# Performance work log

Measured on AMD Instinct MI355X. Metric: run time of the kernel, lower is better.

## Reference

```python
import jax, jax.numpy as jnp
import numpy as np
import math

B, S, D = 2, 2048, 2048
H = 16
HD = D // H          # 128
LAT = 512            # latent_dim


def setup_inputs() -> dict:
    key = jax.random.key(0)
    ks = jax.random.split(key, 8)
    x = jax.random.normal(ks[0], (B, S, D), dtype=jnp.float32)
    freqs = jax.random.uniform(ks[1], (S, HD // 2), dtype=jnp.float32) * (2 * math.pi)
    # additive causal mask: 0 on/below diagonal, -1e9 above
    causal = jnp.tril(jnp.ones((S, S), dtype=bool))
    mask = jnp.where(causal, 0.0, -1e9).astype(jnp.float32)
    sc = 0.02
    Wq = jax.random.normal(ks[2], (D, H * HD), dtype=jnp.float32) * sc
    Wdown = jax.random.normal(ks[3], (D, LAT), dtype=jnp.float32) * sc
    Wkup = jax.random.normal(ks[4], (LAT, H * HD), dtype=jnp.float32) * sc
    Wvup = jax.random.normal(ks[5], (LAT, H * HD), dtype=jnp.float32) * sc
    Wo = jax.random.normal(ks[6], (D, D), dtype=jnp.float32) * sc
    return {"x": x, "freqs": freqs, "mask": mask,
            "Wq": Wq, "Wdown": Wdown, "Wkup": Wkup, "Wvup": Wvup, "Wo": Wo}


def _apply_rope(t, cos, sin):
    # t: [B, S, H, HD]; cos/sin: [1, S, 1, HD//2]
    tp = t.reshape(t.shape[:-1] + (HD // 2, 2))
    t0, t1 = tp[..., 0], tp[..., 1]
    rot = jnp.stack([t0 * cos - t1 * sin, t0 * sin + t1 * cos], axis=-1)
    return rot.reshape(t.shape)


def reference(x, freqs, mask, Wq, Wdown, Wkup, Wvup, Wo):
    b, s, d = x.shape
    Q = (x @ Wq).reshape(b, s, H, HD)
    c_kv = x @ Wdown                       # [B, S, LAT] low-rank latent
    K = (c_kv @ Wkup).reshape(b, s, H, HD)
    V = (c_kv @ Wvup).reshape(b, s, H, HD)
    cos = jnp.cos(freqs)[None, :, None, :]
    sin = jnp.sin(freqs)[None, :, None, :]
    Q = _apply_rope(Q, cos, sin)
    K = _apply_rope(K, cos, sin)
    scores = jnp.einsum('bqhd,bkhd->bhqk', Q, K) / math.sqrt(HD)
    scores = scores + mask                 # [S,S] broadcast over [B,H,S,S]
    probs = jax.nn.softmax(scores, axis=-1)
    attn = jnp.einsum('bhqk,bkhd->bqhd', probs, V).reshape(b, s, d)
    return attn @ Wo
```

## Files before the change

kernel.cpp:

```cpp
#include <hip/hip_runtime.h>
#include <hip/hip_bf16.h>
#include <math.h>

typedef __hip_bfloat16 bf16;
typedef __attribute__((ext_vector_type(8))) short short8;
typedef __attribute__((ext_vector_type(4))) float f32x4;

static constexpr int BB   = 2;
static constexpr int SS   = 2048;
static constexpr int DD   = 2048;
static constexpr int NH   = 16;
static constexpr int HDD  = 128;
static constexpr int LATD = 512;
static constexpr int MR   = BB * SS;
static constexpr int QRS  = DD + LATD;

#if __has_builtin(__builtin_amdgcn_exp2f)
#define EXP2F(x) __builtin_amdgcn_exp2f(x)
#else
#define EXP2F(x) exp2f(x)
#endif

__device__ __forceinline__ void async_cp16(const void* g, void* l) {
    __builtin_amdgcn_global_load_lds(
        (const __attribute__((address_space(1))) void*)g,
        (__attribute__((address_space(3))) void*)l, 16, 0, 0);
}

__device__ __forceinline__ unsigned short bf_bits(bf16 v) {
    union { bf16 b; unsigned short u; } cv; cv.b = v; return cv.u;
}

template <int CTRL>
__device__ __forceinline__ float dpp_mov(float x) {
    int r = __builtin_amdgcn_update_dpp(0, __float_as_int(x), CTRL, 0xF, 0xF, true);
    return __int_as_float(r);
}
__device__ __forceinline__ float dpp_max16(float x) {
    x = fmaxf(x, dpp_mov<0xB1>(x));
    x = fmaxf(x, dpp_mov<0x4E>(x));
    x = fmaxf(x, dpp_mov<0x141>(x));
    x = fmaxf(x, dpp_mov<0x140>(x));
    return x;
}
__device__ __forceinline__ float dpp_sum16(float x) {
    x += dpp_mov<0xB1>(x);
    x += dpp_mov<0x4E>(x);
    x += dpp_mov<0x141>(x);
    x += dpp_mov<0x140>(x);
    return x;
}

__global__ void cast_f32_bf16(const float4* __restrict__ in,
                              ushort4* __restrict__ out, int n4) {
    int i = blockIdx.x * blockDim.x + threadIdx.x;
    if (i >= n4) return;
    float4 v = in[i];
    ushort4 o;
    o.x = bf_bits(__float2bfloat16(v.x));
    o.y = bf_bits(__float2bfloat16(v.y));
    o.z = bf_bits(__float2bfloat16(v.z));
    o.w = bf_bits(__float2bfloat16(v.w));
    out[i] = o;
}

__global__ void transpose_cast(const float* __restrict__ in,
                               bf16* __restrict__ out, int rows, int cols) {
    __shared__ float tile[32][33];
    int tx = threadIdx.x & 31, ty = threadIdx.x >> 5;
    int c0 = blockIdx.x * 32, r0 = blockIdx.y * 32;
    for (int i = 0; i < 32; i += 8)
        tile[ty + i][tx] = in[(size_t)(r0 + ty + i) * cols + c0 + tx];
    __syncthreads();
    for (int i = 0; i < 32; i += 8)
        out[(size_t)(c0 + ty + i) * rows + r0 + tx] =
            __float2bfloat16(tile[tx][ty + i]);
}

__global__ void transpose_v(const bf16* __restrict__ KV, bf16* __restrict__ VT) {
    __shared__ bf16 t[64][74];
    const int tid = threadIdx.x;
    const int s0 = blockIdx.x * 64, d0 = blockIdx.y * 64;
    const int bh = blockIdx.z, b = bh >> 4, h = bh & 15;
    const bf16* src = KV + (size_t)b * SS * 4096 + 2048 + h * 128 + d0;
    for (int p = 0; p < 2; ++p) {
        const int s = p * 32 + (tid >> 3), dc = (tid & 7) * 8;
        short8 v = *(const short8*)(src + (size_t)(s0 + s) * 4096 + dc);
        const bf16* ve = (const bf16*)&v;
        for (int e = 0; e < 8; ++e) t[s][dc + e] = ve[e];
    }
    __syncthreads();
    bf16* dst = VT + ((size_t)bh * HDD + d0) * SS + s0;
    for (int p = 0; p < 2; ++p) {
        const int d = p * 32 + (tid >> 3), g = tid & 7;
        short8 v; bf16* ve = (bf16*)&v;
        for (int e = 0; e < 8; ++e) ve[e] = t[g * 8 + e][d];
        const int gp = g ^ (d & 7);
        *(short8*)(dst + (size_t)d * SS + gp * 8) = v;
    }
}

template <bool OUT_F32>
__global__ __launch_bounds__(256) void gemm_bt(
    const bf16* __restrict__ A, const bf16* __restrict__ Bt,
    void* __restrict__ Cout, int M, int N, int K, int lda, int ldb, int ldc) {
    __shared__ bf16 As[2][128 * 32];
    __shared__ bf16 Bs[2][128 * 32];
    const int tid  = threadIdx.x;
    const int lane = tid & 63, wave = tid >> 6;
    const int quad = lane >> 4, l16 = lane & 15;
    const int row0 = blockIdx.y * 128, col0 = blockIdx.x * 128;
    const int wm = (wave >> 1) * 64, wn = (wave & 1) * 64;
    const int srow = lane >> 2;
    const int scol = (lane & 3) * 8;

    f32x4 acc[4][4];
    for (int i = 0; i < 4; ++i)
        for (int j = 0; j < 4; ++j)
            for (int r = 0; r < 4; ++r) acc[i][j][r] = 0.f;

    auto stage = [&](int k0, int bufi) {
        for (int c = 0; c < 2; ++c) {
            const int chunk = wave * 2 + c;
            const int r = chunk * 16 + srow;
            async_cp16(A  + (size_t)(row0 + r) * lda + k0 + scol, &As[bufi][chunk * 512]);
            async_cp16(Bt + (size_t)(col0 + r) * ldb + k0 + scol, &Bs[bufi][chunk * 512]);
        }
    };

    const int nk = K / 32;
    stage(0, 0);
    for (int ki = 0; ki < nk; ++ki) {
        __syncthreads();
        if (ki + 1 < nk) stage((ki + 1) * 32, (ki + 1) & 1);
        const int bi = ki & 1;
        short8 af[4], bfr[4];
        for (int t = 0; t < 4; ++t) {
            af[t]  = *(const short8*)&As[bi][(wm + t * 16 + l16) * 32 + quad * 8];
            bfr[t] = *(const short8*)&Bs[bi][(wn + t * 16 + l16) * 32 + quad * 8];
        }
        for (int i = 0; i < 4; ++i)
            for (int j = 0; j < 4; ++j)
                acc[i][j] = __builtin_amdgcn_mfma_f32_16x16x32_bf16(
                    af[i], bfr[j], acc[i][j], 0, 0, 0);
    }

    const int rbase = row0 + wm + quad * 4;
    const int cbase = col0 + wn + l16;
    if (OUT_F32) {
        float* C = (float*)Cout;
        for (int i = 0; i < 4; ++i)
            for (int j = 0; j < 4; ++j)
                for (int r = 0; r < 4; ++r)
                    C[(size_t)(rbase + i * 16 + r) * ldc + cbase + j * 16] = acc[i][j][r];
    } else {
        bf16* C = (bf16*)Cout;
        for (int i = 0; i < 4; ++i)
            for (int j = 0; j < 4; ++j)
                for (int r = 0; r < 4; ++r)
                    C[(size_t)(rbase + i * 16 + r) * ldc + cbase + j * 16] =
                        __float2bfloat16(acc[i][j][r]);
    }
}

__global__ void rope_qk(bf16* __restrict__ Q, bf16* __restrict__ KV,
                        const float* __restrict__ freqs, int n) {
    const float QS = 0.08838834764831845f * 1.4426950408889634f;
    int idx = blockIdx.x * blockDim.x + threadIdx.x;
    if (idx >= n) return;
    const int pg  = idx & 15;
    const int h   = (idx >> 4) & (NH - 1);
    const int tok = idx >> 8;
    const int s   = tok & (SS - 1);
    const float4 f = *(const float4*)&freqs[s * 64 + pg * 4];
    float cs[4], sn[4];
    cs[0] = __cosf(f.x); sn[0] = __sinf(f.x);
    cs[1] = __cosf(f.y); sn[1] = __sinf(f.y);
    cs[2] = __cosf(f.z); sn[2] = __sinf(f.z);
    cs[3] = __cosf(f.w); sn[3] = __sinf(f.w);

    bf16* qp = Q  + (size_t)tok * QRS  + h * HDD + pg * 8;
    bf16* kp = KV + (size_t)tok * 4096 + h * HDD + pg * 8;
    for (int pass = 0; pass < 2; ++pass) {
        bf16* p = pass ? kp : qp;
        const float g = pass ? 1.f : QS;
        short8 v = *(const short8*)p;
        const bf16* ve = (const bf16*)&v;
        short8 o;
        bf16* oe = (bf16*)&o;
        for (int i = 0; i < 4; ++i) {
            float t0 = __bfloat162float(ve[2 * i]);
            float t1 = __bfloat162float(ve[2 * i + 1]);
            oe[2 * i]     = __float2bfloat16((t0 * cs[i] - t1 * sn[i]) * g);
            oe[2 * i + 1] = __float2bfloat16((t0 * sn[i] + t1 * cs[i]) * g);
        }
        *(short8*)p = o;
    }
}

__global__ __launch_bounds__(512, 4) void flash_attn(
    const bf16* __restrict__ QC, const bf16* __restrict__ KV,
    const bf16* __restrict__ VTg, bf16* __restrict__ O) {
    const int j = blockIdx.x;
    const int bh = (j >> 3) & 31, q3 = j & 7;
    const int qt = (j & 256) ? q3 : 15 - q3;
    const int h = bh & (NH - 1), b = bh >> 4;
    const int q0 = qt * 128;
    const int tid = threadIdx.x, lane = tid & 63, wave = tid >> 6;
    const int quad = lane >> 4, l16 = lane & 15;

    __shared__ char smem[81920];
    bf16* KsB = (bf16*)smem;
    bf16* VtB = (bf16*)(smem + 32768);
    bf16* PsB = (bf16*)(smem + 65536);

    const bf16* Kb  = KV  + (size_t)b * SS * 4096 + h * HDD;
    const bf16* VTb = VTg + (size_t)bh * HDD * SS;
    const int krs = 4096;

    short8 qf[4];
    {
        const bf16* qrow = QC + (size_t)(b * SS + q0 + wave * 16 + l16) * QRS + h * HDD;
        for (int kk = 0; kk < 4; ++kk)
            qf[kk] = *(const short8*)(qrow + kk * 32 + quad * 8);
    }

    auto stage = [&](int kt, int bufi) {
        const int k0 = kt * 64;
        const int kk = wave >> 1, half = wave & 1;
        for (int i = 0; i < 2; ++i) {
            const int rbase = half * 32 + i * 16;
            async_cp16(Kb + (size_t)(k0 + rbase + (lane >> 2)) * krs
                           + kk * 32 + (lane & 3) * 8,
                       &KsB[bufi * 8192 + kk * 2048 + rbase * 32]);
        }
        for (int c2 = 0; c2 < 2; ++c2) {
            const int c = wave * 2 + c2;
            async_cp16(VTb + (size_t)(c * 8 + (lane >> 3)) * SS + k0 + (lane & 7) * 8,
                       &VtB[bufi * 8192 + c * 512]);
        }
    };

    f32x4 accO[8];
    for (int i = 0; i < 8; ++i)
        for (int r = 0; r < 4; ++r) accO[i][r] = 0.f;
    float m_r[4], l_r[4];
    for (int r = 0; r < 4; ++r) { m_r[r] = -1e30f; l_r[r] = 0.f; }

    const int ktMax = 2 * qt + 1;
    const int qwTop = q0 + wave * 16 + 15;

    stage(0, 0);
    for (int kt = 0; kt <= ktMax; ++kt) {
        const int k0 = kt * 64;
        __syncthreads();
        if (kt < ktMax) stage(kt + 1, (kt + 1) & 1);
        const int bi = kt & 1;

        if (k0 > qwTop) continue;

        f32x4 sfr[4];
        for (int nt = 0; nt < 4; ++nt)
            for (int r = 0; r < 4; ++r) sfr[nt][r] = 0.f;
        for (int kk = 0; kk < 4; ++kk)
            for (int nt = 0; nt < 4; ++nt) {
                short8 kf = *(const short8*)
                    &KsB[bi * 8192 + kk * 2048 + (nt * 16 + l16) * 32 + quad * 8];
                sfr[nt] = __builtin_amdgcn_mfma_f32_16x16x32_bf16(
                    qf[kk], kf, sfr[nt], 0, 0, 0);
            }

        float sv[4][4];
        for (int nt = 0; nt < 4; ++nt)
            for (int r = 0; r < 4; ++r) sv[nt][r] = sfr[nt][r];
        if (kt >= 2 * qt) {
            const int qg = q0 + wave * 16 + quad * 4;
            for (int nt = 0; nt < 4; ++nt) {
                const int kgl = k0 + nt * 16 + l16;
                for (int r = 0; r < 4; ++r)
                    if (kgl > qg + r) sv[nt][r] = -1e30f;
            }
        }
        float rmax[4], alpha[4], psum[4];
        for (int r = 0; r < 4; ++r) {
            float m = fmaxf(fmaxf(sv[0][r], sv[1][r]), fmaxf(sv[2][r], sv[3][r]));
            rmax[r] = dpp_max16(m);
        }
        for (int r = 0; r < 4; ++r) {
            const float mnew = fmaxf(m_r[r], rmax[r]);
            alpha[r] = EXP2F(m_r[r] - mnew);
            m_r[r] = mnew;
        }
        for (int r = 0; r < 4; ++r) psum[r] = 0.f;
        for (int nt = 0; nt < 4; ++nt)
            for (int r = 0; r < 4; ++r) {
                const float p = EXP2F(sv[nt][r] - m_r[r]);
                sv[nt][r] = p;
                psum[r] += p;
            }
        for (int r = 0; r < 4; ++r) {
            psum[r] = dpp_sum16(psum[r]);
            l_r[r] = l_r[r] * alpha[r] + psum[r];
        }
        for (int nt = 0; nt < 8; ++nt)
            for (int r = 0; r < 4; ++r) accO[nt][r] *= alpha[r];

        for (int nt = 0; nt < 4; ++nt)
            for (int r = 0; r < 4; ++r) {
                const int row = quad * 4 + r;
                const int g = nt * 2 + (l16 >> 3);
                PsB[wave * 1024 + row * 64 + ((g ^ (row & 7)) << 3) + (l16 & 7)] =
                    __float2bfloat16(sv[nt][r]);
            }
        __builtin_amdgcn_s_waitcnt(0xc07f);

        for (int ks = 0; ks < 2; ++ks) {
            const int gp = ((ks * 4 + quad) ^ (l16 & 7)) << 3;
            short8 pf = *(const short8*)&PsB[wave * 1024 + l16 * 64 + gp];
            for (int nt = 0; nt < 8; ++nt) {
                const int d = nt * 16 + l16;
                short8 vf = *(const short8*)&VtB[bi * 8192 + d * 64 + gp];
                accO[nt] = __builtin_amdgcn_mfma_f32_16x16x32_bf16(
                    pf, vf, accO[nt], 0, 0, 0);
            }
        }
        __builtin_amdgcn_s_waitcnt(0xc07f);
    }

    bf16* Ob = O + (size_t)b * SS * DD + h * HDD;
    float inv[4];
    for (int r = 0; r < 4; ++r) inv[r] = 1.f / l_r[r];
    for (int nt = 0; nt < 8; ++nt)
        for (int r = 0; r < 4; ++r)
            Ob[(size_t)(q0 + wave * 16 + quad * 4 + r) * DD + nt * 16 + l16] =
                __float2bfloat16(accO[nt][r] * inv[r]);
}

extern "C" void kernel_launch(void* const* d_in, const int* in_sizes, int n_in,
                              void* d_out, int out_size, void* d_ws, size_t ws_size,
                              hipStream_t stream) {
    (void)in_sizes; (void)n_in; (void)out_size; (void)ws_size;
    const float* x     = (const float*)d_in[0];
    const float* freqs = (const float*)d_in[1];
    const float* Wq    = (const float*)d_in[3];
    const float* Wdown = (const float*)d_in[4];
    const float* Wkup  = (const float*)d_in[5];
    const float* Wvup  = (const float*)d_in[6];
    const float* Wo    = (const float*)d_in[7];
    float* out = (float*)d_out;

    char* ws = (char*)d_ws;
    size_t off = 0;
    auto take = [&](size_t bytes) -> void* {
        void* p = ws + off;
        off += (bytes + 255) & ~(size_t)255;
        return p;
    };
    bf16* xb    = (bf16*)take((size_t)MR * DD * 2);
    bf16* WqdT  = (bf16*)take((size_t)QRS * DD * 2);
    bf16* WkvT  = (bf16*)take((size_t)2 * DD * LATD * 2);
    bf16* QC    = (bf16*)take((size_t)MR * QRS * 2);
    bf16* KVb   = (bf16*)take((size_t)MR * 2 * DD * 2);
    bf16* VTg   = (bf16*)take((size_t)BB * NH * HDD * SS * 2);
    bf16* attn  = xb;
    bf16* WoT   = WqdT;

    cast_f32_bf16<<<(MR * DD / 4) / 256, 256, 0, stream>>>(
        (const float4*)x, (ushort4*)xb, MR * DD / 4);

    transpose_cast<<<dim3(DD / 32, DD / 32), 256, 0, stream>>>(Wq, WqdT, DD, DD);
    transpose_cast<<<dim3(LATD / 32, DD / 32), 256, 0, stream>>>(
        Wdown, WqdT + (size_t)DD * DD, DD, LATD);
    transpose_cast<<<dim3(DD / 32, LATD / 32), 256, 0, stream>>>(Wkup, WkvT, LATD, DD);
    transpose_cast<<<dim3(DD / 32, LATD / 32), 256, 0, stream>>>(
        Wvup, WkvT + (size_t)DD * LATD, LATD, DD);

    gemm_bt<false><<<dim3(QRS / 128, MR / 128), 256, 0, stream>>>(
        xb, WqdT, QC, MR, QRS, DD, DD, DD, QRS);
    gemm_bt<false><<<dim3(2 * DD / 128, MR / 128), 256, 0, stream>>>(
        QC + DD, WkvT, KVb, MR, 2 * DD, LATD, QRS, LATD, 2 * DD);

    transpose_v<<<dim3(SS / 64, HDD / 64, BB * NH), 256, 0, stream>>>(KVb, VTg);

    rope_qk<<<(MR * NH * 16) / 256, 256, 0, stream>>>(QC, KVb, freqs, MR * NH * 16);

    flash_attn<<<512, 512, 0, stream>>>(QC, KVb, VTg, attn);

    transpose_cast<<<dim3(DD / 32, DD / 32), 256, 0, stream>>>(Wo, WoT, DD, DD);
    gemm_bt<true><<<dim3(DD / 128, MR / 128), 256, 0, stream>>>(
        attn, WoT, out, MR, DD, DD, DD, DD, DD);
}
```

Measured before the change: 376.4 us.

## Merge prep kernels, fuse Q RoPE into attention, add lazy softmax rescale

The x cast and the four weight transposes become one `prep` launch. The V transpose, K RoPE and Wo transpose become one `tvrope` launch, which cuts launch count and lets small kernels overlap. Q RoPE and scaling now run inside `flash_attn` as Q is loaded into registers, removing a read-modify-write pass over Q. The online softmax skips rescaling `accO` and `l` unless some row max grows by more than 8 in the log2 domain. It also gains hoisted K/V staging addresses and `s_setprio` around the MFMA loops. The lazy rescale lets unnormalised probabilities reach up to 2^8 before bf16 conversion, which changes rounding slightly but stays within range.

```diff
diff --git a/kernel.cpp b/kernel.cpp
--- a/kernel.cpp
+++ b/kernel.cpp
@@ -51,53 +51,46 @@
     return x;
 }
 
-__global__ void cast_f32_bf16(const float4* __restrict__ in,
-                              ushort4* __restrict__ out, int n4) {
-    int i = blockIdx.x * blockDim.x + threadIdx.x;
-    if (i >= n4) return;
-    float4 v = in[i];
-    ushort4 o;
-    o.x = bf_bits(__float2bfloat16(v.x));
-    o.y = bf_bits(__float2bfloat16(v.y));
-    o.z = bf_bits(__float2bfloat16(v.z));
-    o.w = bf_bits(__float2bfloat16(v.w));
-    out[i] = o;
-}
-
-__global__ void transpose_cast(const float* __restrict__ in,
-                               bf16* __restrict__ out, int rows, int cols) {
+__global__ __launch_bounds__(256) void prep(
+    const float* __restrict__ x, bf16* __restrict__ xb,
+    const float* __restrict__ Wq, const float* __restrict__ Wdown,
+    const float* __restrict__ Wkup, const float* __restrict__ Wvup,
+    bf16* __restrict__ WqdT, bf16* __restrict__ WkvT) {
     __shared__ float tile[32][33];
-    int tx = threadIdx.x & 31, ty = threadIdx.x >> 5;
-    int c0 = blockIdx.x * 32, r0 = blockIdx.y * 32;
+    const int blk = blockIdx.x, tid = threadIdx.x;
+    if (blk < 8192) {
+        const int i = blk * 256 + tid;
+        float4 v = ((const float4*)x)[i];
+        ushort4 o;
+        o.x = bf_bits(__float2bfloat16(v.x));
+        o.y = bf_bits(__float2bfloat16(v.y));
+        o.z = bf_bits(__float2bfloat16(v.z));
+        o.w = bf_bits(__float2bfloat16(v.w));
+        ((ushort4*)xb)[i] = o;
+        return;
+    }
+    const float* in; bf16* out; int rows, cols, bx, by;
+    if (blk < 12288) {
+        const int l = blk - 8192;  in = Wq;    out = WqdT;
+        rows = DD;   cols = DD;    bx = l & 63; by = l >> 6;
+    } else if (blk < 13312) {
+        const int l = blk - 12288; in = Wdown; out = WqdT + (size_t)DD * DD;
+        rows = DD;   cols = LATD;  bx = l & 15; by = l >> 4;
+    } else if (blk < 14336) {
+        const int l = blk - 13312; in = Wkup;  out = WkvT;
+        rows = LATD; cols = DD;    bx = l & 63; by = l >> 6;
+    } else {
+        const int l = blk - 14336; in = Wvup;  out = WkvT + (size_t)DD * LATD;
+        rows = LATD; cols = DD;    bx = l & 63; by = l >> 6;
+    }
+    const int tx = tid & 31, ty = tid >> 5;
+    const int c0 = bx * 32, r0 = by * 32;
     for (int i = 0; i < 32; i += 8)
         tile[ty + i][tx] = in[(size_t)(r0 + ty + i) * cols + c0 + tx];
     __syncthreads();
     for (int i = 0; i < 32; i += 8)
         out[(size_t)(c0 + ty + i) * rows + r0 + tx] =
             __float2bfloat16(tile[tx][ty + i]);
-}
-
-__global__ void transpose_v(const bf16* __restrict__ KV, bf16* __restrict__ VT) {
-    __shared__ bf16 t[64][74];
-    const int tid = threadIdx.x;
-    const int s0 = blockIdx.x * 64, d0 = blockIdx.y * 64;
-    const int bh = blockIdx.z, b = bh >> 4, h = bh & 15;
-    const bf16* src = KV + (size_t)b * SS * 4096 + 2048 + h * 128 + d0;
-    for (int p = 0; p < 2; ++p) {
-        const int s = p * 32 + (tid >> 3), dc = (tid & 7) * 8;
-        short8 v = *(const short8*)(src + (size_t)(s0 + s) * 4096 + dc);
-        const bf16* ve = (const bf16*)&v;
-        for (int e = 0; e < 8; ++e) t[s][dc + e] = ve[e];
-    }
-    __syncthreads();
-    bf16* dst = VT + ((size_t)bh * HDD + d0) * SS + s0;
-    for (int p = 0; p < 2; ++p) {
-        const int d = p * 32 + (tid >> 3), g = tid & 7;
-        short8 v; bf16* ve = (bf16*)&v;
-        for (int e = 0; e < 8; ++e) ve[e] = t[g * 8 + e][d];
-        const int gp = g ^ (d & 7);
-        *(short8*)(dst + (size_t)d * SS + gp * 8) = v;
-    }
 }
 
 template <bool OUT_F32>
@@ -163,44 +156,76 @@
     }
 }
 
-__global__ void rope_qk(bf16* __restrict__ Q, bf16* __restrict__ KV,
-                        const float* __restrict__ freqs, int n) {
-    const float QS = 0.08838834764831845f * 1.4426950408889634f;
-    int idx = blockIdx.x * blockDim.x + threadIdx.x;
-    if (idx >= n) return;
-    const int pg  = idx & 15;
-    const int h   = (idx >> 4) & (NH - 1);
-    const int tok = idx >> 8;
-    const int s   = tok & (SS - 1);
-    const float4 f = *(const float4*)&freqs[s * 64 + pg * 4];
-    float cs[4], sn[4];
-    cs[0] = __cosf(f.x); sn[0] = __sinf(f.x);
-    cs[1] = __cosf(f.y); sn[1] = __sinf(f.y);
-    cs[2] = __cosf(f.z); sn[2] = __sinf(f.z);
-    cs[3] = __cosf(f.w); sn[3] = __sinf(f.w);
-
-    bf16* qp = Q  + (size_t)tok * QRS  + h * HDD + pg * 8;
-    bf16* kp = KV + (size_t)tok * 4096 + h * HDD + pg * 8;
-    for (int pass = 0; pass < 2; ++pass) {
-        bf16* p = pass ? kp : qp;
-        const float g = pass ? 1.f : QS;
-        short8 v = *(const short8*)p;
+__global__ __launch_bounds__(256) void tvrope(
+    bf16* __restrict__ KV, bf16* __restrict__ VT,
+    const float* __restrict__ freqs,
+    const float* __restrict__ Wo, bf16* __restrict__ WoT) {
+    __shared__ __align__(16) char sm[64 * 74 * 2];
+    const int blk = blockIdx.x, tid = threadIdx.x;
+    if (blk < 2048) {
+        bf16 (*t)[74] = (bf16(*)[74])sm;
+        const int bx = blk & 31, byy = (blk >> 5) & 1, bh = blk >> 6;
+        const int s0 = bx * 64, d0 = byy * 64;
+        const int b = bh >> 4, h = bh & 15;
+        const bf16* src = KV + (size_t)b * SS * 4096 + 2048 + h * 128 + d0;
+        for (int p = 0; p < 2; ++p) {
+            const int s = p * 32 + (tid >> 3), dc = (tid & 7) * 8;
+            short8 v = *(const short8*)(src + (size_t)(s0 + s) * 4096 + dc);
+            const bf16* ve = (const bf16*)&v;
+            for (int e = 0; e < 8; ++e) t[s][dc + e] = ve[e];
+        }
+        __syncthreads();
+        bf16* dst = VT + ((size_t)bh * HDD + d0) * SS + s0;
+        for (int p = 0; p < 2; ++p) {
+            const int d = p * 32 + (tid >> 3), g = tid & 7;
+            short8 v; bf16* ve = (bf16*)&v;
+            for (int e = 0; e < 8; ++e) ve[e] = t[g * 8 + e][d];
+            const int gp = g ^ (d & 7);
+            *(short8*)(dst + (size_t)d * SS + gp * 8) = v;
+        }
+        return;
+    }
+    if (blk < 6144) {
+        const int idx = (blk - 2048) * 256 + tid;
+        const int pg  = idx & 15;
+        const int h   = (idx >> 4) & (NH - 1);
+        const int tok = idx >> 8;
+        const int s   = tok & (SS - 1);
+        const float4 f = *(const float4*)&freqs[s * 64 + pg * 4];
+        const float fr[4] = {f.x, f.y, f.z, f.w};
+        bf16* kp = KV + (size_t)tok * 4096 + h * HDD + pg * 8;
+        short8 v = *(const short8*)kp;
         const bf16* ve = (const bf16*)&v;
-        short8 o;
-        bf16* oe = (bf16*)&o;
+        short8 o; bf16* oe = (bf16*)&o;
         for (int i = 0; i < 4; ++i) {
-            float t0 = __bfloat162float(ve[2 * i]);
-            float t1 = __bfloat162float(ve[2 * i + 1]);
-            oe[2 * i]     = __float2bfloat16((t0 * cs[i] - t1 * sn[i]) * g);
-            oe[2 * i + 1] = __float2bfloat16((t0 * sn[i] + t1 * cs[i]) * g);
-        }
-        *(short8*)p = o;
+            const float cs = __cosf(fr[i]), sn = __sinf(fr[i]);
+            const float t0 = __bfloat162float(ve[2 * i]);
+            const float t1 = __bfloat162float(ve[2 * i + 1]);
+            oe[2 * i]     = __float2bfloat16(t0 * cs - t1 * sn);
+            oe[2 * i + 1] = __float2bfloat16(t0 * sn + t1 * cs);
+        }
+        *(short8*)kp = o;
+        return;
+    }
+    {
+        float (*tile)[33] = (float(*)[33])sm;
+        const int l = blk - 6144;
+        const int bx = l & 63, by = l >> 6;
+        const int tx = tid & 31, ty = tid >> 5;
+        const int c0 = bx * 32, r0 = by * 32;
+        for (int i = 0; i < 32; i += 8)
+            tile[ty + i][tx] = Wo[(size_t)(r0 + ty + i) * DD + c0 + tx];
+        __syncthreads();
+        for (int i = 0; i < 32; i += 8)
+            WoT[(size_t)(c0 + ty + i) * DD + r0 + tx] =
+                __float2bfloat16(tile[tx][ty + i]);
     }
 }
 
 __global__ __launch_bounds__(512, 4) void flash_attn(
     const bf16* __restrict__ QC, const bf16* __restrict__ KV,
-    const bf16* __restrict__ VTg, bf16* __restrict__ O) {
+    const bf16* __restrict__ VTg, const float* __restrict__ freqs,
+    bf16* __restrict__ O) {
     const int j = blockIdx.x;
     const int bh = (j >> 3) & 31, q3 = j & 7;
     const int qt = (j & 256) ? q3 : 15 - q3;
@@ -218,27 +243,41 @@
     const bf16* VTb = VTg + (size_t)bh * HDD * SS;
     const int krs = 4096;
 
+    const float QS = 0.08838834764831845f * 1.4426950408889634f;
     short8 qf[4];
     {
-        const bf16* qrow = QC + (size_t)(b * SS + q0 + wave * 16 + l16) * QRS + h * HDD;
-        for (int kk = 0; kk < 4; ++kk)
-            qf[kk] = *(const short8*)(qrow + kk * 32 + quad * 8);
-    }
+        const int s = q0 + wave * 16 + l16;
+        const bf16* qrow = QC + (size_t)(b * SS + s) * QRS + h * HDD;
+        for (int kk = 0; kk < 4; ++kk) {
+            short8 v = *(const short8*)(qrow + kk * 32 + quad * 8);
+            const float4 f = *(const float4*)&freqs[s * 64 + kk * 16 + quad * 4];
+            const float fr[4] = {f.x, f.y, f.z, f.w};
+            const bf16* ve = (const bf16*)&v;
+            bf16* oe = (bf16*)&qf[kk];
+            for (int i = 0; i < 4; ++i) {
+                const float cs = __cosf(fr[i]), sn = __sinf(fr[i]);
+                const float t0 = __bfloat162float(ve[2 * i]);
+                const float t1 = __bfloat162float(ve[2 * i + 1]);
+                oe[2 * i]     = __float2bfloat16((t0 * cs - t1 * sn) * QS);
+                oe[2 * i + 1] = __float2bfloat16((t0 * sn + t1 * cs) * QS);
+            }
+        }
+    }
+
+    const int kk_s = wave >> 1, half_s = wave & 1;
+    const bf16* Ksrc = Kb + ((size_t)(half_s * 32) + (lane >> 2)) * krs
+                          + kk_s * 32 + (lane & 3) * 8;
+    const bf16* Vsrc = VTb + ((size_t)(wave * 16) + (lane >> 3)) * SS + (lane & 7) * 8;
 
     auto stage = [&](int kt, int bufi) {
+        const size_t koffK = (size_t)kt * 64 * krs;
         const int k0 = kt * 64;
-        const int kk = wave >> 1, half = wave & 1;
-        for (int i = 0; i < 2; ++i) {
-            const int rbase = half * 32 + i * 16;
-            async_cp16(Kb + (size_t)(k0 + rbase + (lane >> 2)) * krs
-                           + kk * 32 + (lane & 3) * 8,
-                       &KsB[bufi * 8192 + kk * 2048 + rbase * 32]);
-        }
-        for (int c2 = 0; c2 < 2; ++c2) {
-            const int c = wave * 2 + c2;
-            async_cp16(VTb + (size_t)(c * 8 + (lane >> 3)) * SS + k0 + (lane & 7) * 8,
-                       &VtB[bufi * 8192 + c * 512]);
-        }
+        for (int i = 0; i < 2; ++i)
+            async_cp16(Ksrc + koffK + (size_t)i * 16 * krs,
+                       &KsB[bufi * 8192 + kk_s * 2048 + (half_s * 32 + i * 16) * 32]);
+        for (int c2 = 0; c2 < 2; ++c2)
+            async_cp16(Vsrc + (size_t)c2 * 8 * SS + k0,
+                       &VtB[bufi * 8192 + (wave * 2 + c2) * 512]);
     };
 
     f32x4 accO[8];
@@ -262,6 +301,7 @@
         f32x4 sfr[4];
         for (int nt = 0; nt < 4; ++nt)
             for (int r = 0; r < 4; ++r) sfr[nt][r] = 0.f;
+        __builtin_amdgcn_s_setprio(1);
         for (int kk = 0; kk < 4; ++kk)
             for (int nt = 0; nt < 4; ++nt) {
                 short8 kf = *(const short8*)
@@ -269,6 +309,7 @@
                 sfr[nt] = __builtin_amdgcn_mfma_f32_16x16x32_bf16(
                     qf[kk], kf, sfr[nt], 0, 0, 0);
             }
+        __builtin_amdgcn_s_setprio(0);
 
         float sv[4][4];
         for (int nt = 0; nt < 4; ++nt)
@@ -281,29 +322,32 @@
                     if (kgl > qg + r) sv[nt][r] = -1e30f;
             }
         }
-        float rmax[4], alpha[4], psum[4];
+        float rmax[4];
         for (int r = 0; r < 4; ++r) {
             float m = fmaxf(fmaxf(sv[0][r], sv[1][r]), fmaxf(sv[2][r], sv[3][r]));
             rmax[r] = dpp_max16(m);
         }
-        for (int r = 0; r < 4; ++r) {
-            const float mnew = fmaxf(m_r[r], rmax[r]);
-            alpha[r] = EXP2F(m_r[r] - mnew);
-            m_r[r] = mnew;
-        }
-        for (int r = 0; r < 4; ++r) psum[r] = 0.f;
+        const bool grow = (rmax[0] > m_r[0] + 8.f) || (rmax[1] > m_r[1] + 8.f) ||
+                          (rmax[2] > m_r[2] + 8.f) || (rmax[3] > m_r[3] + 8.f);
+        if (__any(grow)) {
+            float alpha[4];
+            for (int r = 0; r < 4; ++r) {
+                const float mnew = fmaxf(m_r[r], rmax[r]);
+                alpha[r] = EXP2F(m_r[r] - mnew);
+                m_r[r] = mnew;
+                l_r[r] *= alpha[r];
+            }
+            for (int nt = 0; nt < 8; ++nt)
+                for (int r = 0; r < 4; ++r) accO[nt][r] *= alpha[r];
+        }
+        float psum[4] = {0.f, 0.f, 0.f, 0.f};
         for (int nt = 0; nt < 4; ++nt)
             for (int r = 0; r < 4; ++r) {
                 const float p = EXP2F(sv[nt][r] - m_r[r]);
                 sv[nt][r] = p;
                 psum[r] += p;
             }
-        for (int r = 0; r < 4; ++r) {
-            psum[r] = dpp_sum16(psum[r]);
-            l_r[r] = l_r[r] * alpha[r] + psum[r];
-        }
-        for (int nt = 0; nt < 8; ++nt)
-            for (int r = 0; r < 4; ++r) accO[nt][r] *= alpha[r];
+        for (int r = 0; r < 4; ++r) l_r[r] += dpp_sum16(psum[r]);
 
         for (int nt = 0; nt < 4; ++nt)
             for (int r = 0; r < 4; ++r) {
@@ -314,6 +358,7 @@
             }
         __builtin_amdgcn_s_waitcnt(0xc07f);
 
+        __builtin_amdgcn_s_setprio(1);
         for (int ks = 0; ks < 2; ++ks) {
             const int gp = ((ks * 4 + quad) ^ (l16 & 7)) << 3;
             short8 pf = *(const short8*)&PsB[wave * 1024 + l16 * 64 + gp];
@@ -324,6 +369,7 @@
                     pf, vf, accO[nt], 0, 0, 0);
             }
         }
+        __builtin_amdgcn_s_setprio(0);
         __builtin_amdgcn_s_waitcnt(0xc07f);
     }
 
@@ -365,28 +411,17 @@
     bf16* attn  = xb;
     bf16* WoT   = WqdT;
 
-    cast_f32_bf16<<<(MR * DD / 4) / 256, 256, 0, stream>>>(
-        (const float4*)x, (ushort4*)xb, MR * DD / 4);
-
-    transpose_cast<<<dim3(DD / 32, DD / 32), 256, 0, stream>>>(Wq, WqdT, DD, DD);
-    transpose_cast<<<dim3(LATD / 32, DD / 32), 256, 0, stream>>>(
-        Wdown, WqdT + (size_t)DD * DD, DD, LATD);
-    transpose_cast<<<dim3(DD / 32, LATD / 32), 256, 0, stream>>>(Wkup, WkvT, LATD, DD);
-    transpose_cast<<<dim3(DD / 32, LATD / 32), 256, 0, stream>>>(
-        Wvup, WkvT + (size_t)DD * LATD, LATD, DD);
+    prep<<<15360, 256, 0, stream>>>(x, xb, Wq, Wdown, Wkup, Wvup, WqdT, WkvT);
 
     gemm_bt<false><<<dim3(QRS / 128, MR / 128), 256, 0, stream>>>(
         xb, WqdT, QC, MR, QRS, DD, DD, DD, QRS);
     gemm_bt<false><<<dim3(2 * DD / 128, MR / 128), 256, 0, stream>>>(
         QC + DD, WkvT, KVb, MR, 2 * DD, LATD, QRS, LATD, 2 * DD);
 
-    transpose_v<<<dim3(SS / 64, HDD / 64, BB * NH), 256, 0, stream>>>(KVb, VTg);
-
-    rope_qk<<<(MR * NH * 16) / 256, 256, 0, stream>>>(QC, KVb, freqs, MR * NH * 16);
-
-    flash_attn<<<512, 512, 0, stream>>>(QC, KVb, VTg, attn);
-
-    transpose_cast<<<dim3(DD / 32, DD / 32), 256, 0, stream>>>(Wo, WoT, DD, DD);
+    tvrope<<<10240, 256, 0, stream>>>(KVb, VTg, freqs, Wo, WoT);
+
+    flash_attn<<<512, 512, 0, stream>>>(QC, KVb, VTg, freqs, attn);
+
     gemm_bt<true><<<dim3(DD / 128, MR / 128), 256, 0, stream>>>(
         attn, WoT, out, MR, DD, DD, DD, DD, DD);
 }
```

After: 347.2 us. -7.8%, faster.
